# Optimization experiments

Hardware: AMD Instinct MI355X
Metric: run time of the kernel (lower is better)

Reference implementation:

```python
import jax, jax.numpy as jnp
import numpy as np

B = 64
HIST_LEN, PRED_HORIZON = 10, 10
H = W = 200
RES = 0.1
INIT_X_IDX, INIT_Y_IDX = 100.0, 160.0
FRONT_EDGE, BACK_EDGE = 3.89, 1.043
HALF_BOX = (FRONT_EDGE + BACK_EDGE) / 2.0
CENTER_SHIFT = HALF_BOX - BACK_EDGE          # mid-circle shift along box heading
FRONT_SHIFT = 2.0 * HALF_BOX - 2.0 * BACK_EDGE
EMBED, HIDDEN, CNN_OUT, CNN_CH = 64, 128, 1000, 32
SIGMA = 1.8
THETA = 0.0


def setup_inputs() -> dict:
    key = jax.random.key(0)
    ks = jax.random.split(key, 16)
    def rn(k, shape, scale=0.02):
        return jax.random.normal(k, shape, dtype=jnp.float32) * scale
    return {
        "img_feature": jax.random.normal(ks[0], (B, 12, H, W), dtype=jnp.float32),
        "hist_points": rn(ks[1], (B, HIST_LEN, 4), 1.0),
        "hist_points_step": rn(ks[2], (B, HIST_LEN, 4), 0.1),
        "ego_rendering_heading": jax.random.uniform(ks[3], (B, 1), dtype=jnp.float32, maxval=2.0 * np.pi),
        "comp_w": rn(ks[4], (3, 12, 3, 3)),
        "comp_b": jnp.zeros((3,), jnp.float32),
        "cnn_w": rn(ks[5], (CNN_CH, 3, 3, 3)),
        "cnn_b": jnp.zeros((CNN_CH,), jnp.float32),
        "cnn_fc_w": rn(ks[6], (CNN_OUT, CNN_CH)),
        "cnn_fc_b": jnp.zeros((CNN_OUT,), jnp.float32),
        "embed_w": rn(ks[7], (EMBED, 4)),
        "embed_b": jnp.zeros((EMBED,), jnp.float32),
        "h0": rn(ks[8], (1, HIDDEN)),
        "c0": rn(ks[9], (1, HIDDEN)),
        "w_ih": rn(ks[10], (4 * HIDDEN, EMBED)),
        "w_hh": rn(ks[11], (4 * HIDDEN, HIDDEN)),
        "b_ih": jnp.zeros((4 * HIDDEN,), jnp.float32),
        "b_hh": jnp.zeros((4 * HIDDEN,), jnp.float32),
        "out_w": rn(ks[12], (4, HIDDEN + CNN_OUT)),
        "out_b": jnp.zeros((4,), jnp.float32),
    }


def _conv(x, w, b, stride):
    y = jax.lax.conv_general_dilated(x, w, (stride, stride), 'SAME',
                                     dimension_numbers=('NCHW', 'OIHW', 'NCHW'))
    return y + b[None, :, None, None]


def _forward(img_feature, hist_points, hist_points_step, ego_rendering_heading,
             comp_w, comp_b, cnn_w, cnn_b, cnn_fc_w, cnn_fc_b,
             embed_w, embed_b, h0, c0, w_ih, w_hh, b_ih, b_hh, out_w, out_b):
    bsz = img_feature.shape[0]
    # CNN encoder: 12->3 compression conv, then backbone (stand-in for mobilenet_v2) -> 1000-dim
    z = _conv(img_feature, comp_w, comp_b, 1)
    z = jax.nn.relu(_conv(z, cnn_w, cnn_b, 2))
    z = z.mean(axis=(2, 3))                       # (B, CNN_CH) global avg pool
    img_emb = z @ cnn_fc_w.T + cnn_fc_b           # (B, 1000)

    def lstm_cell(e, h, c):                       # pytorch gate order i, f, g, o
        g = e @ w_ih.T + b_ih + h @ w_hh.T + b_hh
        i, f, gg, o = jnp.split(g, 4, axis=-1)
        c2 = jax.nn.sigmoid(f) * c + jax.nn.sigmoid(i) * jnp.tanh(gg)
        return jax.nn.sigmoid(o) * jnp.tanh(c2), c2

    def embed(step):
        return jax.nn.relu(step @ embed_w.T + embed_b)

    h = jnp.tile(h0, (bsz, 1))
    c = jnp.tile(c0, (bsz, 1))

    # warm up LSTM on history displacements (torch loop t = 1 .. HIST_LEN-1)
    def hist_step(carry, step_t):
        h, c = carry
        h, c = lstm_cell(embed(step_t), h, c)
        return (h, c), None
    (h, c), _ = jax.lax.scan(hist_step, (h, c),
                             jnp.swapaxes(hist_points_step[:, 1:HIST_LEN], 0, 1))

    def pred_step(carry, _):
        h, c, pose = carry
        step = jnp.concatenate([h, img_emb], axis=1) @ out_w.T + out_b
        pose = pose + step
        h, c = lstm_cell(embed(step), h, c)
        return (h, c, pose), pose
    _, poses = jax.lax.scan(pred_step, (h, c, hist_points[:, HIST_LEN - 1]),
                            None, length=PRED_HORIZON)
    pred_traj = jnp.swapaxes(poses, 0, 1)         # (B, T, 4) == torch pred_traj[:, 1:, :]

    # three-circle gaussian rasterization, vectorized over all timesteps
    ego = ego_rendering_heading.reshape(bsz)      # (B,)
    x, y, hd = pred_traj[..., 0], pred_traj[..., 1], pred_traj[..., 2]
    box_heading = -hd - ego[:, None]              # (B, T)
    ho = -(ego - np.pi / 2.0)                     # heading_offset, (B,)
    cos_ho, sin_ho = jnp.cos(ho)[:, None], jnp.sin(ho)[:, None]
    px = INIT_X_IDX + (x * cos_ho - y * sin_ho) / RES   # rear center in image idx
    py = INIT_Y_IDX - (x * sin_ho + y * cos_ho) / RES
    cos_bh, sin_bh = jnp.cos(box_heading), jnp.sin(box_heading)

    # idx_mesh built with meshgrid indexing='ij' over (W, H); image is square
    gx, gy = jnp.meshgrid(jnp.arange(W, dtype=jnp.float32),
                          jnp.arange(H, dtype=jnp.float32), indexing='ij')
    ct, st = np.cos(THETA), np.sin(THETA)
    ga = ct * ct / (2 * SIGMA ** 2) + st * st / (2 * SIGMA ** 2)
    gb = -np.sin(2 * THETA) / (4 * SIGMA ** 2) + np.sin(2 * THETA) / (4 * SIGMA ** 2)
    gc = st * st / (2 * SIGMA ** 2) + ct * ct / (2 * SIGMA ** 2)

    def gauss(shift):
        cx = px + shift / RES * cos_bh            # (B, T)
        cy = py - shift / RES * sin_bh
        dx = gx[None, None] - cx[..., None, None] # (B, T, H, W)
        dy = gy[None, None] - cy[..., None, None]
        return jnp.exp(-(ga * dx * dx + 2 * gb * dx * dy + gc * dy * dy))

    boxes = jnp.maximum(gauss(0.0), jnp.maximum(gauss(CENTER_SHIFT), gauss(FRONT_SHIFT)))
    pred_boxs = boxes[:, :, None]                 # (B, T, 1, H, W)
    return pred_traj, pred_boxs


def reference(img_feature, hist_points, hist_points_step, ego_rendering_heading,
              comp_w, comp_b, cnn_w, cnn_b, cnn_fc_w, cnn_fc_b,
              embed_w, embed_b, h0, c0, w_ih, w_hh, b_ih, b_hh, out_w, out_b):
    return _forward(img_feature, hist_points, hist_points_step, ego_rendering_heading,
                    comp_w, comp_b, cnn_w, cnn_b, cnn_fc_w, cnn_fc_b,
                    embed_w, embed_b, h0, c0, w_ih, w_hh, b_ih, b_hh, out_w, out_b)
```

## Files before the change

### kernel.cpp

```cpp
#include <hip/hip_runtime.h>
#include <math.h>

typedef _Float16 f16;
typedef f16 f16x2 __attribute__((ext_vector_type(2)));
typedef f16 f16x4 __attribute__((ext_vector_type(4)));

__device__ __forceinline__ float dot2acc(f16x2 a, f16x2 b, float c){
#if __has_builtin(__builtin_amdgcn_fdot2)
  return __builtin_amdgcn_fdot2(a, b, c, false);
#else
  return c + (float)a[0]*(float)b[0] + (float)a[1]*(float)b[1];
#endif
}

__global__ __launch_bounds__(256) void k_conv1(const float* __restrict__ img,
    const float* __restrict__ cw, const float* __restrict__ cb,
    f16* __restrict__ c1h){
  int b = blockIdx.y, ty = blockIdx.x;
  int t = threadIdx.x, lane = t & 63, wv = t >> 6;
  int y0 = ty*5;

  __shared__ __align__(16) float sbuf[2][3072];

  int goff[3];
  #pragma unroll
  for (int j=0;j<3;++j){
    int k = wv + 4*j;
    int e = k*64 + lane; if (e > 699) e = 699;
    int ch = e/350, rem = e - 350*ch;
    int lr = rem/50, c4 = rem - 50*lr;
    int gy = y0 - 1 + lr; gy = gy < 0 ? 0 : (gy > 199 ? 199 : gy);
    goff[j] = ch*40000 + gy*200 + c4*4;
  }
  const float* cbase0 = img + (size_t)b*480000;

  int cg = t % 50, r = t / 50;
  int y = y0 + r;
  bool rok[3];
  #pragma unroll
  for (int rr=0; rr<3; ++rr) rok[rr] = (unsigned)(y-1+rr) < 200u;
  bool xl = (cg>0), xr = (cg<49);

  float acc[3][4];
  #pragma unroll
  for (int oc=0;oc<3;++oc){
    float bz = cb[oc];
    #pragma unroll
    for (int c=0;c<4;++c) acc[oc][c] = bz;
  }

  auto STAGE = [&](int buf, int p){
    const float* cp = cbase0 + p*80000;
    #pragma unroll
    for (int j=0;j<3;++j){
      int k = wv + 4*j;
      const float* g = cp + goff[j];
#if __has_builtin(__builtin_amdgcn_global_load_lds)
      __builtin_amdgcn_global_load_lds(
          (const __attribute__((address_space(1))) void*)g,
          (__attribute__((address_space(3))) void*)&sbuf[buf][k*256], 16, 0, 0);
#else
      *(float4*)&sbuf[buf][(k*64 + lane)*4] = *(const float4*)g;
#endif
    }
  };

  STAGE(0, 0);
  for (int p=0; p<6; ++p){
    int cur = p & 1;
    if (p < 5){
      STAGE(cur^1, p+1);
      asm volatile("s_waitcnt vmcnt(3)" ::: "memory");
    } else {
      asm volatile("s_waitcnt vmcnt(0)" ::: "memory");
    }
    __builtin_amdgcn_s_barrier();
    if (t < 250){
      #pragma unroll
      for (int cc=0; cc<2; ++cc){
        float vr[3][6];
        #pragma unroll
        for (int rr=0; rr<3; ++rr){
          const float* rp = &sbuf[cur][cc*1400 + (r+rr)*200 + 4*cg];
          if (rok[rr]){
            float4 m = *(const float4*)rp;
            vr[rr][0] = xl ? rp[-1] : 0.f;
            vr[rr][1] = m.x; vr[rr][2] = m.y; vr[rr][3] = m.z; vr[rr][4] = m.w;
            vr[rr][5] = xr ? rp[4] : 0.f;
          } else {
            #pragma unroll
            for (int q=0;q<6;++q) vr[rr][q] = 0.f;
          }
        }
        int ci = 2*p + cc;
        #pragma unroll
        for (int oc=0;oc<3;++oc){
          const float* wp = cw + oc*108 + ci*9;
          float w00=wp[0], w01=wp[1], w02=wp[2],
                w10=wp[3], w11=wp[4], w12=wp[5],
                w20=wp[6], w21=wp[7], w22=wp[8];
          #pragma unroll
          for (int c=0;c<4;++c){
            float s = acc[oc][c];
            s = fmaf(vr[0][c+0], w00, s); s = fmaf(vr[0][c+1], w01, s); s = fmaf(vr[0][c+2], w02, s);
            s = fmaf(vr[1][c+0], w10, s); s = fmaf(vr[1][c+1], w11, s); s = fmaf(vr[1][c+2], w12, s);
            s = fmaf(vr[2][c+0], w20, s); s = fmaf(vr[2][c+1], w21, s); s = fmaf(vr[2][c+2], w22, s);
            acc[oc][c] = s;
          }
        }
      }
    }
    __builtin_amdgcn_s_barrier();
  }

  if (t < 250){
    f16* ob = c1h + (size_t)b*120000;
    #pragma unroll
    for (int oc=0;oc<3;++oc){
      f16x4 w4;
      #pragma unroll
      for (int c=0;c<4;++c) w4[c] = (f16)acc[oc][c];
      *(f16x4*)(ob + oc*40000 + y*200 + 4*cg) = w4;
    }
  }
}

__global__ __launch_bounds__(256) void k_conv2(const f16* __restrict__ c1h,
    const float* __restrict__ w2, const float* __restrict__ b2,
    float* __restrict__ part){
  int b = blockIdx.y, ty = blockIdx.x;
  int t = threadIdx.x, lane = t&63, wv = t>>6;
  __shared__ __align__(16) f16 z[6656];
  const f16* cbs = c1h + (size_t)b*120000;

  #pragma unroll
  for (int j=0;j<4;++j){
    int k = wv + 4*j;
    int e = k*64 + lane;
    if (e < 825){
      int ci = e/275, rem = e - 275*ci;
      int lr = rem/25, c8 = (rem - 25*lr)*8;
      int gy = 10*ty - 1 + lr; if (gy < 0) gy = 0;
      const f16* g = cbs + ci*40000 + gy*200 + c8;
#if __has_builtin(__builtin_amdgcn_global_load_lds)
      __builtin_amdgcn_global_load_lds(
          (const __attribute__((address_space(1))) void*)g,
          (__attribute__((address_space(3))) void*)&z[k*512], 16, 0, 0);
#else
      *(float4*)&z[e*8] = *(const float4*)g;
#endif
    }
  }
  __syncthreads();

  float acc[32];
  #pragma unroll
  for (int co=0;co<32;++co) acc[co]=0.f;
  if (t < 250){
    int r = t/50;
    int g = t%50;
    bool xl = (g>0);
    float vr[3][3][5];
    #pragma unroll
    for (int ci=0;ci<3;++ci){
      #pragma unroll
      for (int ky=0;ky<3;++ky){
        int s = 2*r + ky;
        bool rok = (10*ty + 2*r + ky - 1) >= 0;
        const f16* rp = &z[ci*2200 + s*200 + 4*g];
        if (rok){
          f16x4 m = *(const f16x4*)rp;
          vr[ci][ky][0] = xl ? (float)rp[-1] : 0.f;
          vr[ci][ky][1] = (float)m[0]; vr[ci][ky][2] = (float)m[1];
          vr[ci][ky][3] = (float)m[2]; vr[ci][ky][4] = (float)m[3];
        } else {
          #pragma unroll
          for (int q=0;q<5;++q) vr[ci][ky][q] = 0.f;
        }
      }
    }
    #pragma unroll
    for (int c=0;c<2;++c){
      #pragma unroll
      for (int co=0;co<32;++co){
        float s = b2[co];
        #pragma unroll
        for (int ci=0;ci<3;++ci)
          #pragma unroll
          for (int ky=0;ky<3;++ky)
            #pragma unroll
            for (int kx=0;kx<3;++kx)
              s = fmaf(vr[ci][ky][2*c+kx], w2[co*27+ci*9+ky*3+kx], s);
        acc[co] += fmaxf(s, 0.f);
      }
    }
  }
  __shared__ float wred[4][32];
  #pragma unroll
  for (int co=0;co<32;++co){
    float s = acc[co];
    #pragma unroll
    for (int off=32; off; off>>=1) s += __shfl_down(s, off, 64);
    if (lane==0) wred[wv][co] = s;
  }
  __syncthreads();
  if (t < 32){
    float s = wred[0][t]+wred[1][t]+wred[2][t]+wred[3][t];
    part[(b*20+ty)*32 + t] = s;
  }
}

__global__ __launch_bounds__(256) void k_lstm(
    const float* __restrict__ hist_pts, const float* __restrict__ hist_step,
    const float* __restrict__ emb_w, const float* __restrict__ emb_b,
    const float* __restrict__ h0, const float* __restrict__ c0,
    const float* __restrict__ w_ih, const float* __restrict__ w_hh,
    const float* __restrict__ b_ih, const float* __restrict__ b_hh,
    const float* __restrict__ out_w, const float* __restrict__ out_b,
    const float* __restrict__ part, const float* __restrict__ fcw,
    const float* __restrict__ fcb, float* __restrict__ traj){
  int b = blockIdx.x; int t = threadIdx.x; int lane = t&63, wv = t>>6;

  __shared__ float zfc[32];
  __shared__ float wredfc[4][4];
  if (t < 32){
    float s = 0.f;
    #pragma unroll
    for (int p=0;p<20;++p) s += part[(b*20+p)*32 + t];
    zfc[t] = s * (1.f/10000.f);
  }
  __syncthreads();
  {
    float cp0=0.f, cp1=0.f, cp2=0.f, cp3=0.f;
    for (int o = t; o < 1000; o += 256){
      float s = fcb[o];
      #pragma unroll
      for (int k=0;k<32;++k) s = fmaf(fcw[o*32+k], zfc[k], s);
      cp0 = fmaf(s, out_w[0*1128+128+o], cp0);
      cp1 = fmaf(s, out_w[1*1128+128+o], cp1);
      cp2 = fmaf(s, out_w[2*1128+128+o], cp2);
      cp3 = fmaf(s, out_w[3*1128+128+o], cp3);
    }
    #pragma unroll
    for (int off=32; off; off>>=1){
      cp0 += __shfl_down(cp0, off, 64);
      cp1 += __shfl_down(cp1, off, 64);
      cp2 += __shfl_down(cp2, off, 64);
      cp3 += __shfl_down(cp3, off, 64);
    }
    if (lane==0){ wredfc[wv][0]=cp0; wredfc[wv][1]=cp1; wredfc[wv][2]=cp2; wredfc[wv][3]=cp3; }
  }
  __syncthreads();
  float cst = 0.f;
  if (t < 4) cst = out_b[t] + wredfc[0][t]+wredfc[1][t]+wredfc[2][t]+wredfc[3][t];

  int u  = (t<128) ? t       : t-128;
  int j1 = (t<128) ? t       : 128+u;
  int j2 = (t<128) ? 256+t   : 384+u;

  f16x2 w1[96], w2[96];
  {
    const float2* r1 = (const float2*)(w_ih + j1*64);
    const float2* r2 = (const float2*)(w_ih + j2*64);
    #pragma unroll
    for (int p=0;p<32;++p){
      float2 a = r1[p], c = r2[p];
      w1[p] = f16x2{(f16)a.x, (f16)a.y};
      w2[p] = f16x2{(f16)c.x, (f16)c.y};
    }
    const float2* q1 = (const float2*)(w_hh + j1*128);
    const float2* q2 = (const float2*)(w_hh + j2*128);
    #pragma unroll
    for (int p=0;p<64;++p){
      float2 a = q1[p], c = q2[p];
      w1[32+p] = f16x2{(f16)a.x, (f16)a.y};
      w2[32+p] = f16x2{(f16)c.x, (f16)c.y};
    }
  }
  float bias1 = b_ih[j1] + b_hh[j1];
  float bias2 = b_ih[j2] + b_hh[j2];

  __shared__ f16x2 xl[96];
  __shared__ float e_lds[64], h_lds[128], a_lds[128];
  __shared__ float step_lds[4], wred4[4];

  float c_reg = (t>=128) ? c0[u] : 0.f;
  if (t < 128) h_lds[t] = h0[t];

  auto cell = [&](){
    __syncthreads();
    if (t < 32)      xl[t]    = f16x2{(f16)e_lds[2*t],        (f16)e_lds[2*t+1]};
    else if (t < 96){ int p=t-32; xl[t] = f16x2{(f16)h_lds[2*p], (f16)h_lds[2*p+1]}; }
    __syncthreads();
    float acc1 = bias1, acc2 = bias2;
    #pragma unroll
    for (int cc=0; cc<12; ++cc){
      f16x2 xv[8];
      #pragma unroll
      for (int q=0;q<8;++q) xv[q] = xl[cc*8+q];
      #pragma unroll
      for (int q=0;q<8;++q){
        acc1 = dot2acc(w1[cc*8+q], xv[q], acc1);
        acc2 = dot2acc(w2[cc*8+q], xv[q], acc2);
      }
    }
    if (t < 128){
      float ig = 1.f/(1.f+expf(-acc1));
      float gg = tanhf(acc2);
      a_lds[t] = ig*gg;
    }
    __syncthreads();
    if (t >= 128){
      float ff = 1.f/(1.f+expf(-acc1));
      float oo = 1.f/(1.f+expf(-acc2));
      c_reg = ff*c_reg + a_lds[u];
      h_lds[u] = oo * tanhf(c_reg);
    }
  };

  for (int s=1; s<10; ++s){
    if (t < 64){
      const float* hp = hist_step + (size_t)(b*10+s)*4;
      float e = emb_b[t]
              + emb_w[t*4+0]*hp[0] + emb_w[t*4+1]*hp[1]
              + emb_w[t*4+2]*hp[2] + emb_w[t*4+3]*hp[3];
      e_lds[t] = fmaxf(e, 0.f);
    }
    cell();
  }

  float pose = (t<4) ? hist_pts[(size_t)(b*10+9)*4 + t] : 0.f;
  for (int it=0; it<10; ++it){
    __syncthreads();
    {
      const float* owr = out_w + wv*1128;
      float p_ = owr[2*lane]*h_lds[2*lane] + owr[2*lane+1]*h_lds[2*lane+1];
      #pragma unroll
      for (int off=32; off; off>>=1) p_ += __shfl_down(p_, off, 64);
      if (lane==0) wred4[wv] = p_;
    }
    __syncthreads();
    if (t < 4){
      float st = wred4[t] + cst;
      pose += st;
      traj[(size_t)(b*10+it)*4 + t] = pose;
      step_lds[t] = st;
    }
    __syncthreads();
    if (it < 9){
      if (t < 64){
        float e = emb_b[t]
                + emb_w[t*4+0]*step_lds[0] + emb_w[t*4+1]*step_lds[1]
                + emb_w[t*4+2]*step_lds[2] + emb_w[t*4+3]*step_lds[3];
        e_lds[t] = fmaxf(e, 0.f);
      }
      cell();
    }
  }
}

__global__ __launch_bounds__(256) void k_raster(const float* __restrict__ traj,
    const float* __restrict__ ego, float* __restrict__ boxes){
  int img = blockIdx.y;
  int b = img / 10;
  __shared__ float ctr[6];
  if (threadIdx.x == 0){
    float x  = traj[img*4+0];
    float y  = traj[img*4+1];
    float hd = traj[img*4+2];
    float eg = ego[b];
    float ho = 1.5707963267948966f - eg;
    float sho, cho; __sincosf(ho, &sho, &cho);
    float pxc = 100.f + (x*cho - y*sho)*10.f;
    float pyc = 160.f - (x*sho + y*cho)*10.f;
    float bh  = -hd - eg;
    float sbh, cbh; __sincosf(bh, &sbh, &cbh);
    const float CSH = 14.235f;
    const float FSH = 28.47f;
    ctr[0] = pxc;             ctr[1] = pyc;
    ctr[2] = pxc + CSH*cbh;   ctr[3] = pyc - CSH*sbh;
    ctr[4] = pxc + FSH*cbh;   ctr[5] = pyc - FSH*sbh;
  }
  __syncthreads();
  int f4 = blockIdx.x*256 + threadIdx.x;
  if (f4 >= 10000) return;
  int p0 = f4*4;
  int i = p0 / 200;
  int j = p0 % 200;
  float fi = (float)i, fj = (float)j;
  float c0x=ctr[0], c0y=ctr[1], c1x=ctr[2], c1y=ctr[3], c2x=ctr[4], c2y=ctr[5];
  float dx0 = fi-c0x, dx1 = fi-c1x, dx2 = fi-c2x;
  float A0 = dx0*dx0, A1 = dx1*dx1, A2 = dx2*dx2;
  const float GA = 0.15432098765432098f;
  float r[4];
  #pragma unroll
  for (int l=0;l<4;++l){
    float dj = fj + (float)l;
    float dy0 = dj-c0y, dy1 = dj-c1y, dy2 = dj-c2y;
    float d0 = fmaf(dy0,dy0,A0);
    float d1 = fmaf(dy1,dy1,A1);
    float d2 = fmaf(dy2,dy2,A2);
    float m = fminf(d0, fminf(d1,d2));
    r[l] = __expf(-m*GA);
  }
  *(float4*)(boxes + (size_t)img*40000 + p0) = make_float4(r[0],r[1],r[2],r[3]);
}

extern "C" void kernel_launch(void* const* d_in, const int* in_sizes, int n_in,
                              void* d_out, int out_size, void* d_ws, size_t ws_size,
                              hipStream_t stream) {
  (void)in_sizes; (void)n_in; (void)d_ws; (void)ws_size; (void)out_size;
  const float* img = (const float*)d_in[0];
  const float* hp  = (const float*)d_in[1];
  const float* hps = (const float*)d_in[2];
  const float* ego = (const float*)d_in[3];
  const float* cw  = (const float*)d_in[4];
  const float* cb  = (const float*)d_in[5];
  const float* c2w = (const float*)d_in[6];
  const float* c2b = (const float*)d_in[7];
  const float* fcw = (const float*)d_in[8];
  const float* fcb = (const float*)d_in[9];
  const float* ew  = (const float*)d_in[10];
  const float* eb  = (const float*)d_in[11];
  const float* h0  = (const float*)d_in[12];
  const float* c0  = (const float*)d_in[13];
  const float* wih = (const float*)d_in[14];
  const float* whh = (const float*)d_in[15];
  const float* bih = (const float*)d_in[16];
  const float* bhh = (const float*)d_in[17];
  const float* ow  = (const float*)d_in[18];
  const float* ob  = (const float*)d_in[19];

  float* out  = (float*)d_out;
  float* traj = out;
  float* S    = out + 2560;
  float* part = S;
  f16*   c1h  = (f16*)(S + 50000);

  hipLaunchKernelGGL(k_conv1, dim3(40, 64), dim3(256), 0, stream, img, cw, cb, c1h);
  hipLaunchKernelGGL(k_conv2, dim3(20, 64), dim3(256), 0, stream, c1h, c2w, c2b, part);
  hipLaunchKernelGGL(k_lstm,  dim3(64),     dim3(256), 0, stream,
                     hp, hps, ew, eb, h0, c0, wih, whh, bih, bhh, ow, ob, part, fcw, fcb, traj);
  hipLaunchKernelGGL(k_raster, dim3(40, 640), dim3(256), 0, stream, traj, ego, S);
}
```

Before: 138.2 us.

## Stage conv1 input as packed fp16 channel pairs and use dot2 accumulation

The first compression conv no longer stages fp32 tiles into LDS with direct global-to-LDS loads. Each thread now prefetches the next two channels into registers, packs them as fp16 channel pairs into a smaller LDS buffer, and runs the 3x3 taps with fdot2 instead of scalar FMAs. The change also drops the trailing barrier in each iteration and halves the LDS footprint, aiming to cut ALU work and synchronisation. In exchange, the 12-channel input and the weights are rounded to fp16 (round-toward-zero) before accumulation, which reduces precision.

```diff
diff --git a/kernel.cpp b/kernel.cpp
--- a/kernel.cpp
+++ b/kernel.cpp
@@ -13,33 +13,46 @@
 #endif
 }
 
+__device__ __forceinline__ f16x2 pk2(float a, float b){
+#if __has_builtin(__builtin_amdgcn_cvt_pkrtz)
+  auto h = __builtin_amdgcn_cvt_pkrtz(a, b);
+  return *(f16x2*)&h;
+#else
+  return f16x2{(f16)a, (f16)b};
+#endif
+}
+
+union U4 { uint4 u; f16x2 h[4]; };
+
 __global__ __launch_bounds__(256) void k_conv1(const float* __restrict__ img,
     const float* __restrict__ cw, const float* __restrict__ cb,
     f16* __restrict__ c1h){
   int b = blockIdx.y, ty = blockIdx.x;
-  int t = threadIdx.x, lane = t & 63, wv = t >> 6;
+  int t = threadIdx.x;
   int y0 = ty*5;
 
-  __shared__ __align__(16) float sbuf[2][3072];
-
-  int goff[3];
-  #pragma unroll
-  for (int j=0;j<3;++j){
-    int k = wv + 4*j;
-    int e = k*64 + lane; if (e > 699) e = 699;
-    int ch = e/350, rem = e - 350*ch;
-    int lr = rem/50, c4 = rem - 50*lr;
-    int gy = y0 - 1 + lr; gy = gy < 0 ? 0 : (gy > 199 ? 199 : gy);
-    goff[j] = ch*40000 + gy*200 + c4*4;
-  }
-  const float* cbase0 = img + (size_t)b*480000;
+  __shared__ __align__(16) f16x2 sb[2][1408];
+
+  bool has1 = (t < 94);
+  int e1 = t + 256;
+  int lr0 = t/50,  c40 = t%50;
+  int lr1 = e1/50, c41 = e1%50;
+  int gy0 = y0 - 1 + lr0; gy0 = gy0<0?0:(gy0>199?199:gy0);
+  int gy1 = y0 - 1 + lr1; gy1 = gy1<0?0:(gy1>199?199:gy1);
+  int off0 = gy0*200 + c40*4;
+  int off1 = gy1*200 + c41*4;
+  int l0 = lr0*200 + c40*4;
+  int l1 = lr1*200 + c41*4;
+  const float* cb0 = img + (size_t)b*480000;
 
   int cg = t % 50, r = t / 50;
   int y = y0 + r;
+  bool act = (t < 250);
   bool rok[3];
   #pragma unroll
   for (int rr=0; rr<3; ++rr) rok[rr] = (unsigned)(y-1+rr) < 200u;
   bool xl = (cg>0), xr = (cg<49);
+  const f16x2 z2 = f16x2{(f16)0.f,(f16)0.f};
 
   float acc[3][4];
   #pragma unroll
@@ -49,71 +62,78 @@
     for (int c=0;c<4;++c) acc[oc][c] = bz;
   }
 
-  auto STAGE = [&](int buf, int p){
-    const float* cp = cbase0 + p*80000;
-    #pragma unroll
-    for (int j=0;j<3;++j){
-      int k = wv + 4*j;
-      const float* g = cp + goff[j];
-#if __has_builtin(__builtin_amdgcn_global_load_lds)
-      __builtin_amdgcn_global_load_lds(
-          (const __attribute__((address_space(1))) void*)g,
-          (__attribute__((address_space(3))) void*)&sbuf[buf][k*256], 16, 0, 0);
-#else
-      *(float4*)&sbuf[buf][(k*64 + lane)*4] = *(const float4*)g;
-#endif
-    }
-  };
-
-  STAGE(0, 0);
+  float4 A0 = make_float4(0,0,0,0), A1 = A0, B0 = A0, B1 = A0;
+  {
+    const float* cp = cb0;
+    A0 = *(const float4*)(cp + off0); A1 = *(const float4*)(cp + 40000 + off0);
+    if (has1){ B0 = *(const float4*)(cp + off1); B1 = *(const float4*)(cp + 40000 + off1); }
+  }
+
+  #pragma unroll
   for (int p=0; p<6; ++p){
-    int cur = p & 1;
+    float4 cA0=A0, cA1=A1, cB0=B0, cB1=B1;
     if (p < 5){
-      STAGE(cur^1, p+1);
-      asm volatile("s_waitcnt vmcnt(3)" ::: "memory");
-    } else {
-      asm volatile("s_waitcnt vmcnt(0)" ::: "memory");
-    }
+      const float* cp = cb0 + (p+1)*80000;
+      A0 = *(const float4*)(cp + off0); A1 = *(const float4*)(cp + 40000 + off0);
+      if (has1){ B0 = *(const float4*)(cp + off1); B1 = *(const float4*)(cp + 40000 + off1); }
+    }
+    f16x2* dst = sb[p & 1];
+    {
+      U4 w0;
+      w0.h[0]=pk2(cA0.x,cA1.x); w0.h[1]=pk2(cA0.y,cA1.y);
+      w0.h[2]=pk2(cA0.z,cA1.z); w0.h[3]=pk2(cA0.w,cA1.w);
+      *(uint4*)&dst[l0] = w0.u;
+      if (has1){
+        U4 w1;
+        w1.h[0]=pk2(cB0.x,cB1.x); w1.h[1]=pk2(cB0.y,cB1.y);
+        w1.h[2]=pk2(cB0.z,cB1.z); w1.h[3]=pk2(cB0.w,cB1.w);
+        *(uint4*)&dst[l1] = w1.u;
+      }
+    }
+    asm volatile("s_waitcnt lgkmcnt(0)" ::: "memory");
     __builtin_amdgcn_s_barrier();
-    if (t < 250){
-      #pragma unroll
-      for (int cc=0; cc<2; ++cc){
-        float vr[3][6];
+
+    if (act){
+      f16x2 wpk[3][9];
+      #pragma unroll
+      for (int oc=0;oc<3;++oc)
         #pragma unroll
-        for (int rr=0; rr<3; ++rr){
-          const float* rp = &sbuf[cur][cc*1400 + (r+rr)*200 + 4*cg];
-          if (rok[rr]){
-            float4 m = *(const float4*)rp;
-            vr[rr][0] = xl ? rp[-1] : 0.f;
-            vr[rr][1] = m.x; vr[rr][2] = m.y; vr[rr][3] = m.z; vr[rr][4] = m.w;
-            vr[rr][5] = xr ? rp[4] : 0.f;
-          } else {
-            #pragma unroll
-            for (int q=0;q<6;++q) vr[rr][q] = 0.f;
+        for (int k=0;k<9;++k)
+          wpk[oc][k] = pk2(cw[oc*108 + (2*p)*9 + k], cw[oc*108 + (2*p+1)*9 + k]);
+
+      f16x2 vp[3][6];
+      #pragma unroll
+      for (int rr=0; rr<3; ++rr){
+        const f16x2* rp = &dst[(r+rr)*200 + 4*cg];
+        if (rok[rr]){
+          U4 q; q.u = *(const uint4*)rp;
+          vp[rr][0] = xl ? rp[-1] : z2;
+          vp[rr][1] = q.h[0]; vp[rr][2] = q.h[1];
+          vp[rr][3] = q.h[2]; vp[rr][4] = q.h[3];
+          vp[rr][5] = xr ? rp[4] : z2;
+        } else {
+          #pragma unroll
+          for (int q2=0;q2<6;++q2) vp[rr][q2] = z2;
+        }
+      }
+      #pragma unroll
+      for (int oc=0;oc<3;++oc){
+        #pragma unroll
+        for (int c=0;c<4;++c){
+          float s = acc[oc][c];
+          #pragma unroll
+          for (int ky=0;ky<3;++ky){
+            s = dot2acc(wpk[oc][ky*3+0], vp[ky][c+0], s);
+            s = dot2acc(wpk[oc][ky*3+1], vp[ky][c+1], s);
+            s = dot2acc(wpk[oc][ky*3+2], vp[ky][c+2], s);
           }
+          acc[oc][c] = s;
         }
-        int ci = 2*p + cc;
-        #pragma unroll
-        for (int oc=0;oc<3;++oc){
-          const float* wp = cw + oc*108 + ci*9;
-          float w00=wp[0], w01=wp[1], w02=wp[2],
-                w10=wp[3], w11=wp[4], w12=wp[5],
-                w20=wp[6], w21=wp[7], w22=wp[8];
-          #pragma unroll
-          for (int c=0;c<4;++c){
-            float s = acc[oc][c];
-            s = fmaf(vr[0][c+0], w00, s); s = fmaf(vr[0][c+1], w01, s); s = fmaf(vr[0][c+2], w02, s);
-            s = fmaf(vr[1][c+0], w10, s); s = fmaf(vr[1][c+1], w11, s); s = fmaf(vr[1][c+2], w12, s);
-            s = fmaf(vr[2][c+0], w20, s); s = fmaf(vr[2][c+1], w21, s); s = fmaf(vr[2][c+2], w22, s);
-            acc[oc][c] = s;
-          }
-        }
-      }
-    }
-    __builtin_amdgcn_s_barrier();
-  }
-
-  if (t < 250){
+      }
+    }
+  }
+
+  if (act){
     f16* ob = c1h + (size_t)b*120000;
     #pragma unroll
     for (int oc=0;oc<3;++oc){
```

Result: faster. 133.5 us (-3.4%).
